# Kernel tuning notes

Measured on AMD Instinct MI355X. Metric: run time of the kernel, lower is better.

## Reference

```python
import jax, jax.numpy as jnp
import numpy as np

H = 1024   # hidden_size
B, S, L = 8, 4096, 64


def setup_inputs() -> dict:
    key = jax.random.key(0)
    k1, k2, k3 = jax.random.split(key, 3)
    hidden = jax.random.normal(k1, (L, B, H), dtype=jnp.float32)
    encoder_states = jax.random.normal(k2, (B, S, 2 * H), dtype=jnp.float32)
    # nn.Linear(2H, H): weight [H, 2H], bias [H]
    W = jax.random.normal(k3, (H, 2 * H), dtype=jnp.float32) * (1.0 / np.sqrt(2 * H))
    b = jnp.zeros((H,), dtype=jnp.float32)
    return {"hidden": hidden, "encoder_states": encoder_states, "W": W, "b": b}


def reference(hidden, encoder_states, W, b):
    # fc projection: [B,S,2H] @ [2H,H] -> [B,S,H]
    reduced = jnp.einsum('bsk,hk->bsh', encoder_states, W) + b
    # scores: bmm(reduced [B,S,H], hidden.permute(1,2,0) [B,H,L]) -> [B,S,L]
    scores = jnp.einsum('bsh,lbh->bsl', reduced, hidden)
    # softmax over encoder positions (dim=1)
    weights = jax.nn.softmax(scores, axis=1)
    # context: bmm(weights^T [B,L,S], reduced [B,S,H]) -> [B,L,H]
    context = jnp.einsum('bsl,bsh->blh', weights, reduced)
    return context, weights
```

## Files before the change

### kernel.cpp

```cpp
#include <hip/hip_runtime.h>


#define H_ 1024
#define B_ 8
#define S_ 4096
#define L_ 64
#define K2H 2048

typedef _Float16 f16x8 __attribute__((ext_vector_type(8)));
typedef _Float16 f16x4 __attribute__((ext_vector_type(4)));
typedef float f32x4 __attribute__((ext_vector_type(4)));


__global__ __launch_bounds__(256) void kcast_kernel(const float* __restrict__ src,
                                                    _Float16* __restrict__ hi,
                                                    _Float16* __restrict__ lo) {
    __shared__ float T[16][516];
    const int t = threadIdx.x;
    const int slab = blockIdx.x, ksec = blockIdx.y;
    const float* sp = src + (size_t)slab * 16 * K2H + ksec * 512;
#pragma unroll
    for (int r = 0; r < 8; r++) {
        int lin = r * 1024 + t * 4;
        int row = lin >> 9, col = lin & 511;
        float4 v = *(const float4*)(sp + (size_t)row * K2H + col);
        T[row][col] = v.x; T[row][col + 1] = v.y; T[row][col + 2] = v.z; T[row][col + 3] = v.w;
    }
    __syncthreads();
    const size_t obase = ((size_t)slab * 64 + ksec * 16) * 512;
#pragma unroll
    for (int r = 0; r < 4; r++) {
        int c = r * 256 + t;
        int kt = c >> 6, lam = c & 63;
        int m = lam & 15, kb = kt * 32 + (lam >> 4) * 8;
        f16x8 h, l;
#pragma unroll
        for (int e = 0; e < 8; e++) {
            float x = T[m][kb + e];
            _Float16 hh = (_Float16)x;
            h[e] = hh;
            l[e] = (_Float16)(x - (float)hh);
        }
        *(f16x8*)(hi + obase + (size_t)c * 8) = h;
        if (lo) *(f16x8*)(lo + obase + (size_t)c * 8) = l;
    }
}

__global__ __launch_bounds__(256, 4) void kcs_kernel(const float* __restrict__ enc,
                                                     _Float16* __restrict__ encB,
                                                     const _Float16* __restrict__ vh,
                                                     const _Float16* __restrict__ vl,
                                                     float* __restrict__ scores) {
    __shared__ _Float16 TT[2][16][520];
    const int t = threadIdx.x;
    const int slab = blockIdx.x;
    const int b = slab >> 8;
    const int w = t >> 6, lane = t & 63;
    const int ml = lane & 15, q = lane >> 4;
    f32x4 acc[4] = {};

    const float* sp0 = enc + (size_t)slab * (16 * K2H);
    float4 rbuf[8];
#pragma unroll
    for (int r = 0; r < 8; r++) {
        int lin = r * 1024 + t * 4;
        rbuf[r] = *(const float4*)(sp0 + (size_t)(lin >> 9) * K2H + (lin & 511));
    }
    const int qb = (slab & 1) * 2;
    const int st = (slab & 255) >> 1;

    for (int ksec = 0; ksec < 4; ksec++) {
#pragma unroll
        for (int r = 0; r < 8; r++) {
            int lin = r * 1024 + t * 4;
            int row = lin >> 9, col = lin & 511;
            float4 v = rbuf[r];
            f16x4 h4, l4;
            h4[0] = (_Float16)v.x; h4[1] = (_Float16)v.y;
            h4[2] = (_Float16)v.z; h4[3] = (_Float16)v.w;
            l4[0] = (_Float16)(v.x - (float)h4[0]);
            l4[1] = (_Float16)(v.y - (float)h4[1]);
            l4[2] = (_Float16)(v.z - (float)h4[2]);
            l4[3] = (_Float16)(v.w - (float)h4[3]);
            *(f16x4*)&TT[0][row][col] = h4;
            *(f16x4*)&TT[1][row][col] = l4;
        }
        __syncthreads();
        if (ksec < 3) {
            const float* sp = sp0 + (ksec + 1) * 512;
#pragma unroll
            for (int r = 0; r < 8; r++) {
                int lin = r * 1024 + t * 4;
                rbuf[r] = *(const float4*)(sp + (size_t)(lin >> 9) * K2H + (lin & 511));
            }
        }
#pragma unroll
        for (int p = 0; p < 4; p++) {
            const int pid = p * 256 + t;
            const int ctl = pid >> 5;
            const int w5 = pid & 31;
            const int oct = w5 >> 4, c = w5 & 15;
            f16x8 v;
#pragma unroll
            for (int e = 0; e < 8; e++) v[e] = TT[0][oct * 8 + e][ctl * 16 + c];
            const int ctg = ksec * 32 + ctl;
            const size_t off = (((size_t)(b * 128 + ctg)) * 128 + st) * 512
                             + (size_t)((qb + oct) * 16 + c) * 8;
            *(f16x8*)(encB + off) = v;
        }
#pragma unroll
        for (int r = 0; r < 4; r++) {
            const int ktl = r * 4 + w;
            const int kb = ktl * 32 + q * 8;
            f16x8 h = *(const f16x8*)&TT[0][ml][kb];
            f16x8 l = *(const f16x8*)&TT[1][ml][kb];
            const int ktg = ksec * 16 + ktl;
            const size_t vbase = (((size_t)(b * 4) * 64) + ktg) * 512 + (size_t)lane * 8;
#pragma unroll
            for (int lt = 0; lt < 4; lt++) {
                f16x8 bH = *(const f16x8*)(vh + vbase + (size_t)lt * 32768);
                f16x8 bL = *(const f16x8*)(vl + vbase + (size_t)lt * 32768);
                acc[lt] = __builtin_amdgcn_mfma_f32_16x16x32_f16(h, bH, acc[lt], 0, 0, 0);
                acc[lt] = __builtin_amdgcn_mfma_f32_16x16x32_f16(l, bH, acc[lt], 0, 0, 0);
                acc[lt] = __builtin_amdgcn_mfma_f32_16x16x32_f16(h, bL, acc[lt], 0, 0, 0);
            }
        }
        __syncthreads();
    }
    float (*P)[16][66] = reinterpret_cast<float (*)[16][66]>(&TT[0][0][0]);
#pragma unroll
    for (int lt = 0; lt < 4; lt++)
#pragma unroll
        for (int r = 0; r < 4; r++)
            P[w][q * 4 + r][lt * 16 + ml] = acc[lt][r];
    __syncthreads();
    const int s0 = (slab & 255) * 16;
#pragma unroll
    for (int u = 0; u < 4; u++) {
        const int idx = u * 256 + t;
        const int srow = idx >> 6, l = idx & 63;
        float v = P[0][srow][l] + P[1][srow][l] + P[2][srow][l] + P[3][srow][l];
        scores[(size_t)b * (S_ * L_) + (size_t)(s0 + srow) * L_ + l] = v;
    }
}

__global__ __launch_bounds__(256) void kv2_kernel(const float* __restrict__ hidden,
                                                  const float* __restrict__ W,
                                                  _Float16* __restrict__ vh,
                                                  _Float16* __restrict__ vl) {
    __shared__ float Ah[64][17];
    __shared__ float Wt[16][64];
    const int b = blockIdx.x;
    const int k0 = blockIdx.y * 64;
    const int t = threadIdx.x;
    const int lt = t & 15, kt = t >> 4;
    float acc[4][4];
#pragma unroll
    for (int i = 0; i < 4; i++)
#pragma unroll
        for (int j = 0; j < 4; j++) acc[i][j] = 0.f;

    const int ar = t >> 2, ac4 = (t & 3) * 4;
    const int wrow = t >> 4, wc4 = (t & 15) * 4;

    for (int h0 = 0; h0 < H_; h0 += 16) {
        float4 av = *(const float4*)(hidden + (size_t)ar * (B_ * H_) + b * H_ + h0 + ac4);
        Ah[ar][ac4 + 0] = av.x; Ah[ar][ac4 + 1] = av.y; Ah[ar][ac4 + 2] = av.z; Ah[ar][ac4 + 3] = av.w;
        *(float4*)&Wt[wrow][wc4] = *(const float4*)(W + (size_t)(h0 + wrow) * K2H + k0 + wc4);
        __syncthreads();
#pragma unroll
        for (int hh = 0; hh < 16; hh++) {
            float a0 = Ah[lt * 4 + 0][hh], a1 = Ah[lt * 4 + 1][hh];
            float a2 = Ah[lt * 4 + 2][hh], a3 = Ah[lt * 4 + 3][hh];
            float4 wv = *(const float4*)&Wt[hh][kt * 4];
            acc[0][0] += a0 * wv.x; acc[0][1] += a0 * wv.y; acc[0][2] += a0 * wv.z; acc[0][3] += a0 * wv.w;
            acc[1][0] += a1 * wv.x; acc[1][1] += a1 * wv.y; acc[1][2] += a1 * wv.z; acc[1][3] += a1 * wv.w;
            acc[2][0] += a2 * wv.x; acc[2][1] += a2 * wv.y; acc[2][2] += a2 * wv.z; acc[2][3] += a2 * wv.w;
            acc[3][0] += a3 * wv.x; acc[3][1] += a3 * wv.y; acc[3][2] += a3 * wv.z; acc[3][3] += a3 * wv.w;
        }
        __syncthreads();
    }
#pragma unroll
    for (int i = 0; i < 4; i++) {
        const int l = lt * 4 + i;
        const int ltile = l >> 4, lam = l & 15;
#pragma unroll
        for (int j = 0; j < 4; j++) {
            const int k = k0 + kt * 4 + j;
            const size_t idx = (((size_t)(b * 4 + ltile) * 64) + (k >> 5)) * 512
                             + (size_t)((((k >> 3) & 3) * 16 + lam) * 8 + (k & 7));
            float v = acc[i][j];
            _Float16 hh = (_Float16)v;
            vh[idx] = hh;
            vl[idx] = (_Float16)(v - (float)hh);
        }
    }
}

__global__ __launch_bounds__(256) void kU_kernel(const _Float16* __restrict__ wa,
                                                 const _Float16* __restrict__ encB,
                                                 float* __restrict__ Upart) {
    const int t = threadIdx.x;
    const int b = blockIdx.x, nc = blockIdx.y, ks = blockIdx.z;
    const int w = t >> 6, lane = t & 63;
    const int ml = lane & 15, q = lane >> 4;
    const int wm = w >> 1, wn = w & 1;
    f32x4 acc[2][2] = {};

    for (int it = 0; it < 32; ++it) {
        const int stile = ks * 32 + it;
        f16x8 bf[2];
#pragma unroll
        for (int j = 0; j < 2; j++) {
            const int ct = nc * 4 + wn * 2 + j;
            bf[j] = *(const f16x8*)(encB + (((size_t)(b * 128 + ct)) * 128 + stile) * 512
                                     + (size_t)lane * 8);
        }
#pragma unroll
        for (int i = 0; i < 2; i++) {
            f16x8 a = *(const f16x8*)(wa + (((size_t)(b * 4 + wm * 2 + i)) * 128 + stile) * 512
                                       + (size_t)lane * 8);
#pragma unroll
            for (int j = 0; j < 2; j++)
                acc[i][j] = __builtin_amdgcn_mfma_f32_16x16x32_f16(a, bf[j], acc[i][j], 0, 0, 0);
        }
    }
#pragma unroll
    for (int i = 0; i < 2; i++)
#pragma unroll
        for (int j = 0; j < 2; j++)
#pragma unroll
            for (int r = 0; r < 4; r++) {
                const int l = wm * 32 + i * 16 + q * 4 + r;
                const int ch = nc * 64 + (wn * 2 + j) * 16 + ml;
                Upart[(((size_t)(ks * 8 + b)) * 64 + l) * K2H + ch] = acc[i][j][r];
            }
}

__global__ __launch_bounds__(256) void kC_kernel(const float* __restrict__ Upart,
                                                 const _Float16* __restrict__ w16h,
                                                 const _Float16* __restrict__ w16l,
                                                 const float* __restrict__ bias,
                                                 float* __restrict__ ctx) {
    __shared__ _Float16 AsH[64][40], AsL[64][40];
    const int t = threadIdx.x;
    const int hc = blockIdx.x, b = blockIdx.y, kq = blockIdx.z;
    const int w = t >> 6, lane = t & 63;
    const int ml = lane & 15, q = lane >> 4;
    const int wm = w >> 1, wn = w & 1;
    f32x4 acc[2][2] = {};
    const int r0 = t >> 2, c8 = (t & 3) * 8;

    for (int k0 = kq * 512; k0 < kq * 512 + 512; k0 += 32) {
        float xv[8];
#pragma unroll
        for (int e = 0; e < 8; e++) xv[e] = 0.f;
        const size_t ub = ((size_t)b * 64 + r0) * K2H + k0 + c8;
#pragma unroll
        for (int p = 0; p < 4; p++) {
            const float* up = Upart + (size_t)p * (8 * 64 * K2H) + ub;
            float4 u0 = *(const float4*)up, u1 = *(const float4*)(up + 4);
            xv[0] += u0.x; xv[1] += u0.y; xv[2] += u0.z; xv[3] += u0.w;
            xv[4] += u1.x; xv[5] += u1.y; xv[6] += u1.z; xv[7] += u1.w;
        }
        f16x8 hh, ll;
#pragma unroll
        for (int e = 0; e < 8; e++) {
            _Float16 hv = (_Float16)xv[e];
            hh[e] = hv;
            ll[e] = (_Float16)(xv[e] - (float)hv);
        }
        *(f16x8*)&AsH[r0][c8] = hh;
        *(f16x8*)&AsL[r0][c8] = ll;
        __syncthreads();
        const int kt = k0 >> 5;
        f16x8 bH[2], bL[2];
#pragma unroll
        for (int j = 0; j < 2; j++) {
            const size_t wb = (((size_t)(hc * 4 + wn * 2 + j)) * 64 + kt) * 512 + (size_t)lane * 8;
            bH[j] = *(const f16x8*)(w16h + wb);
            bL[j] = *(const f16x8*)(w16l + wb);
        }
#pragma unroll
        for (int i = 0; i < 2; i++) {
            f16x8 aH = *(const f16x8*)&AsH[wm * 32 + i * 16 + ml][q * 8];
            f16x8 aL = *(const f16x8*)&AsL[wm * 32 + i * 16 + ml][q * 8];
#pragma unroll
            for (int j = 0; j < 2; j++) {
                acc[i][j] = __builtin_amdgcn_mfma_f32_16x16x32_f16(aH, bH[j], acc[i][j], 0, 0, 0);
                acc[i][j] = __builtin_amdgcn_mfma_f32_16x16x32_f16(aL, bH[j], acc[i][j], 0, 0, 0);
                acc[i][j] = __builtin_amdgcn_mfma_f32_16x16x32_f16(aH, bL[j], acc[i][j], 0, 0, 0);
            }
        }
        __syncthreads();
    }
#pragma unroll
    for (int i = 0; i < 2; i++)
#pragma unroll
        for (int j = 0; j < 2; j++) {
            const int h = hc * 64 + wn * 32 + j * 16 + ml;
            const float bv = (kq == 0) ? bias[h] : 0.f;
#pragma unroll
            for (int r = 0; r < 4; r++) {
                const int l = wm * 32 + i * 16 + q * 4 + r;
                atomicAdd(ctx + (((size_t)(b * 64 + l)) << 10) + h, acc[i][j][r] + bv);
            }
        }
}


__global__ __launch_bounds__(256) void ksb_kernel(const float* __restrict__ hidden,
                                                  const float* __restrict__ bias,
                                                  float* __restrict__ sb) {
    const int b = blockIdx.x, t = threadIdx.x;
    const int l = t & 63, j = t >> 6;
    const float* hp = hidden + (size_t)l * (B_ * H_) + b * H_ + j * 256;
    const float* bp = bias + j * 256;
    float s = 0.f;
    for (int i = 0; i < 64; i++) {
        float4 h4 = *(const float4*)(hp + i * 4);
        float4 b4 = *(const float4*)(bp + i * 4);
        s += h4.x * b4.x + h4.y * b4.y + h4.z * b4.z + h4.w * b4.w;
    }
    __shared__ float red[256];
    red[t] = s; __syncthreads();
    if (t < 128) red[t] += red[t + 128];
    __syncthreads();
    if (t < 64) sb[b * 64 + t] = red[t] + red[t + 64];
}

__global__ __launch_bounds__(256) void kv_kernel(const float* __restrict__ hidden,
                                                 const float* __restrict__ W,
                                                 float* __restrict__ V) {
    __shared__ float Ah[64][17];
    __shared__ float Wt[16][64];
    const int b = blockIdx.x;
    const int k0 = blockIdx.y * 64;
    const int t = threadIdx.x;
    const int lt = t & 15, kt = t >> 4;
    float acc[4][4];
#pragma unroll
    for (int i = 0; i < 4; i++)
#pragma unroll
        for (int j = 0; j < 4; j++) acc[i][j] = 0.f;

    const int ar = t >> 2, ac4 = (t & 3) * 4;
    const int wrow = t >> 4, wc4 = (t & 15) * 4;

    for (int h0 = 0; h0 < H_; h0 += 16) {
        float4 av = *(const float4*)(hidden + (size_t)ar * (B_ * H_) + b * H_ + h0 + ac4);
        Ah[ar][ac4 + 0] = av.x; Ah[ar][ac4 + 1] = av.y; Ah[ar][ac4 + 2] = av.z; Ah[ar][ac4 + 3] = av.w;
        *(float4*)&Wt[wrow][wc4] = *(const float4*)(W + (size_t)(h0 + wrow) * K2H + k0 + wc4);
        __syncthreads();
#pragma unroll
        for (int hh = 0; hh < 16; hh++) {
            float a0 = Ah[lt * 4 + 0][hh], a1 = Ah[lt * 4 + 1][hh];
            float a2 = Ah[lt * 4 + 2][hh], a3 = Ah[lt * 4 + 3][hh];
            float4 wv = *(const float4*)&Wt[hh][kt * 4];
            acc[0][0] += a0 * wv.x; acc[0][1] += a0 * wv.y; acc[0][2] += a0 * wv.z; acc[0][3] += a0 * wv.w;
            acc[1][0] += a1 * wv.x; acc[1][1] += a1 * wv.y; acc[1][2] += a1 * wv.z; acc[1][3] += a1 * wv.w;
            acc[2][0] += a2 * wv.x; acc[2][1] += a2 * wv.y; acc[2][2] += a2 * wv.z; acc[2][3] += a2 * wv.w;
            acc[3][0] += a3 * wv.x; acc[3][1] += a3 * wv.y; acc[3][2] += a3 * wv.z; acc[3][3] += a3 * wv.w;
        }
        __syncthreads();
    }
#pragma unroll
    for (int i = 0; i < 4; i++) {
        float4 o; o.x = acc[i][0]; o.y = acc[i][1]; o.z = acc[i][2]; o.w = acc[i][3];
        *(float4*)(V + (size_t)b * (L_ * K2H) + (lt * 4 + i) * K2H + k0 + kt * 4) = o;
    }
}

__global__ __launch_bounds__(256) void k1_kernel(const float* __restrict__ enc,
                                                 const float* __restrict__ W,
                                                 const float* __restrict__ bias,
                                                 _Float16* __restrict__ reduced) {
    __shared__ _Float16 As[128][40];
    __shared__ _Float16 Bs[128][40];
    const int t = threadIdx.x;
    const int n0 = blockIdx.x * 128;
    const int m0 = blockIdx.y * 128;
    const int w = t >> 6, lane = t & 63;
    const int wr = w >> 1, wc = w & 1;
    const int ml = lane & 15, q = lane >> 4;

    f32x4 acc[4][4];
#pragma unroll
    for (int i = 0; i < 4; i++)
#pragma unroll
        for (int j = 0; j < 4; j++) acc[i][j] = (f32x4){0.f, 0.f, 0.f, 0.f};

    const int r0 = t >> 2;
    const int c8 = (t & 3) * 8;

    for (int k0 = 0; k0 < K2H; k0 += 32) {
#pragma unroll
        for (int j = 0; j < 2; ++j) {
            const int row = r0 + 64 * j;
            const float* pa = enc + (size_t)(m0 + row) * K2H + k0 + c8;
            float4 a0 = *(const float4*)pa, a1 = *(const float4*)(pa + 4);
            f16x8 ha;
            ha[0] = (_Float16)a0.x; ha[1] = (_Float16)a0.y; ha[2] = (_Float16)a0.z; ha[3] = (_Float16)a0.w;
            ha[4] = (_Float16)a1.x; ha[5] = (_Float16)a1.y; ha[6] = (_Float16)a1.z; ha[7] = (_Float16)a1.w;
            *(f16x8*)&As[row][c8] = ha;
            const float* pb = W + (size_t)(n0 + row) * K2H + k0 + c8;
            float4 b0 = *(const float4*)pb, b1 = *(const float4*)(pb + 4);
            f16x8 hb;
            hb[0] = (_Float16)b0.x; hb[1] = (_Float16)b0.y; hb[2] = (_Float16)b0.z; hb[3] = (_Float16)b0.w;
            hb[4] = (_Float16)b1.x; hb[5] = (_Float16)b1.y; hb[6] = (_Float16)b1.z; hb[7] = (_Float16)b1.w;
            *(f16x8*)&Bs[row][c8] = hb;
        }
        __syncthreads();
        f16x8 af[4], bf[4];
#pragma unroll
        for (int i = 0; i < 4; i++) af[i] = *(const f16x8*)&As[wr * 64 + i * 16 + ml][q * 8];
#pragma unroll
        for (int j = 0; j < 4; j++) bf[j] = *(const f16x8*)&Bs[wc * 64 + j * 16 + ml][q * 8];
#pragma unroll
        for (int i = 0; i < 4; i++)
#pragma unroll
            for (int j = 0; j < 4; j++)
                acc[i][j] = __builtin_amdgcn_mfma_f32_16x16x32_f16(af[i], bf[j], acc[i][j], 0, 0, 0);
        __syncthreads();
    }
#pragma unroll
    for (int j = 0; j < 4; j++) {
        const int h = n0 + wc * 64 + j * 16 + ml;
        const float bv = bias[h];
#pragma unroll
        for (int i = 0; i < 4; i++) {
            const int srow = m0 + wr * 64 + i * 16 + q * 4;
#pragma unroll
            for (int r = 0; r < 4; r++)
                reduced[(size_t)(srow + r) * H_ + h] = (_Float16)(acc[i][j][r] + bv);
        }
    }
}

__global__ __launch_bounds__(256) void ks_kernel(const float* __restrict__ enc,
                                                 const float* __restrict__ V,
                                                 const float* __restrict__ sb,
                                                 float* __restrict__ scores) {
    __shared__ _Float16 AsH[64][40], AsL[64][40];
    __shared__ _Float16 BsH[64][40], BsL[64][40];
    const int t = threadIdx.x;
    const int s0 = blockIdx.x * 64;
    const int b = blockIdx.y;
    const int w = t >> 6, lane = t & 63;
    const int ml = lane & 15, q = lane >> 4;

    f32x4 acc[4];
#pragma unroll
    for (int j = 0; j < 4; j++) acc[j] = (f32x4){0.f, 0.f, 0.f, 0.f};

    const int r0 = t >> 2, c8 = (t & 3) * 8;

    for (int k0 = 0; k0 < K2H; k0 += 32) {
        {
            const float* pa = enc + (size_t)(b * S_ + s0 + r0) * K2H + k0 + c8;
            float4 a0 = *(const float4*)pa, a1 = *(const float4*)(pa + 4);
            float xv[8] = {a0.x, a0.y, a0.z, a0.w, a1.x, a1.y, a1.z, a1.w};
            f16x8 hh, ll;
#pragma unroll
            for (int e = 0; e < 8; e++) {
                _Float16 hi = (_Float16)xv[e];
                hh[e] = hi;
                ll[e] = (_Float16)(xv[e] - (float)hi);
            }
            *(f16x8*)&AsH[r0][c8] = hh;
            *(f16x8*)&AsL[r0][c8] = ll;
        }
        {
            const float* pb = V + (size_t)b * (L_ * K2H) + (size_t)r0 * K2H + k0 + c8;
            float4 b0 = *(const float4*)pb, b1 = *(const float4*)(pb + 4);
            float xv[8] = {b0.x, b0.y, b0.z, b0.w, b1.x, b1.y, b1.z, b1.w};
            f16x8 hh, ll;
#pragma unroll
            for (int e = 0; e < 8; e++) {
                _Float16 hi = (_Float16)xv[e];
                hh[e] = hi;
                ll[e] = (_Float16)(xv[e] - (float)hi);
            }
            *(f16x8*)&BsH[r0][c8] = hh;
            *(f16x8*)&BsL[r0][c8] = ll;
        }
        __syncthreads();
        f16x8 aH = *(const f16x8*)&AsH[w * 16 + ml][q * 8];
        f16x8 aL = *(const f16x8*)&AsL[w * 16 + ml][q * 8];
#pragma unroll
        for (int j = 0; j < 4; j++) {
            f16x8 bH = *(const f16x8*)&BsH[j * 16 + ml][q * 8];
            f16x8 bL = *(const f16x8*)&BsL[j * 16 + ml][q * 8];
            acc[j] = __builtin_amdgcn_mfma_f32_16x16x32_f16(aH, bH, acc[j], 0, 0, 0);
            acc[j] = __builtin_amdgcn_mfma_f32_16x16x32_f16(aL, bH, acc[j], 0, 0, 0);
            acc[j] = __builtin_amdgcn_mfma_f32_16x16x32_f16(aH, bL, acc[j], 0, 0, 0);
        }
        __syncthreads();
    }
#pragma unroll
    for (int j = 0; j < 4; j++) {
        const int l = j * 16 + ml;
        const float sbv = sb[b * 64 + l];
        const int srow = s0 + w * 16 + q * 4;
#pragma unroll
        for (int r = 0; r < 4; r++)
            scores[(size_t)b * (S_ * L_) + (size_t)(srow + r) * L_ + l] = acc[j][r] + sbv;
    }
}

__global__ __launch_bounds__(256) void k4_kernel(const float* __restrict__ wbuf,
                                                 const _Float16* __restrict__ reduced,
                                                 float* __restrict__ ctx) {
    __shared__ float Ws[64][64];
    __shared__ _Float16 Rs[64][256];
    const int t = threadIdx.x;
    const int b = blockIdx.x, ht = blockIdx.y, sc = blockIdx.z;
    const int h = ht * 256 + t;
    float acc[64];
#pragma unroll
    for (int l = 0; l < 64; l++) acc[l] = 0.f;

    for (int cc = 0; cc < 4; ++cc) {
        const int sbase = sc * 256 + cc * 64;
#pragma unroll
        for (int j = 0; j < 4; j++) {
            int c = t + 256 * j;
            int row = c >> 4, c4 = (c & 15) * 4;
            *(float4*)&Ws[row][c4] =
                *(const float4*)(wbuf + (size_t)b * (S_ * L_) + (size_t)(sbase + row) * L_ + c4);
        }
#pragma unroll
        for (int j = 0; j < 8; j++) {
            int c = t + 256 * j;
            int row = c >> 5, ch = (c & 31) * 8;
            *(uint4*)&Rs[row][ch] =
                *(const uint4*)(reduced + (size_t)(b * S_ + sbase + row) * H_ + ht * 256 + ch);
        }
        __syncthreads();
        for (int ss = 0; ss < 64; ++ss) {
            float r = (float)Rs[ss][t];
            const float4* wr = (const float4*)&Ws[ss][0];
#pragma unroll
            for (int u = 0; u < 16; u++) {
                float4 wv = wr[u];
                acc[u * 4 + 0] += wv.x * r;
                acc[u * 4 + 1] += wv.y * r;
                acc[u * 4 + 2] += wv.z * r;
                acc[u * 4 + 3] += wv.w * r;
            }
        }
        __syncthreads();
    }
#pragma unroll
    for (int l = 0; l < 64; l++)
        atomicAdd(ctx + (size_t)((b * 64 + l) << 10) + h, acc[l]);
}


__global__ __launch_bounds__(256) void k3a_kernel(const float* __restrict__ scores,
                                                  float* __restrict__ partM,
                                                  float* __restrict__ partD) {
    const int b = blockIdx.x, chunk = blockIdx.y;
    const int t = threadIdx.x;
    const int l = t & 63, si = t >> 6;
    const float* p = scores + (size_t)b * (S_ * L_) + (size_t)(chunk * 256 + si * 64) * L_ + l;
    float m = -__builtin_inff(), d = 0.f;
    for (int i = 0; i < 64; i++) {
        float x = p[i * 64];
        if (x > m) { d = d * __expf(m - x) + 1.f; m = x; }
        else d += __expf(x - m);
    }
    __shared__ float sm[256], sd[256];
    sm[t] = m; sd[t] = d; __syncthreads();
    if (t < 128) {
        float m2 = sm[t + 128], d2 = sd[t + 128];
        if (m2 > sm[t]) { sd[t] = sd[t] * __expf(sm[t] - m2) + d2; sm[t] = m2; }
        else sd[t] += d2 * __expf(m2 - sm[t]);
    }
    __syncthreads();
    if (t < 64) {
        float m1 = sm[t], d1 = sd[t], m2 = sm[t + 64], d2 = sd[t + 64];
        if (m2 > m1) { d1 = d1 * __expf(m1 - m2) + d2; m1 = m2; }
        else d1 += d2 * __expf(m2 - m1);
        partM[(b * 16 + chunk) * 64 + t] = m1;
        partD[(b * 16 + chunk) * 64 + t] = d1;
    }
}

__global__ __launch_bounds__(512) void k3b_kernel(const float* __restrict__ partM,
                                                  const float* __restrict__ partD,
                                                  float* __restrict__ fm,
                                                  float* __restrict__ fdinv) {
    const int t = threadIdx.x;
    const int b = t >> 6, l = t & 63;
    float m = -__builtin_inff(), d = 0.f;
    for (int c = 0; c < 16; c++) {
        float pm = partM[(b * 16 + c) * 64 + l];
        float pd = partD[(b * 16 + c) * 64 + l];
        if (pm > m) { d = d * __expf(m - pm) + pd; m = pm; }
        else d += pd * __expf(pm - m);
    }
    fm[t] = m;
    fdinv[t] = 1.0f / d;
}

__global__ __launch_bounds__(256) void k3c_kernel(float* __restrict__ wbuf,
                                                  const float* __restrict__ fm,
                                                  const float* __restrict__ fdinv,
                                                  _Float16* __restrict__ watile) {
    const int t = threadIdx.x;
    const int l = t & 63;
    const int g = blockIdx.x * 4 + (t >> 6);
    const int b = g >> 9;
    const int s0 = (g & 511) * 8;
    const float m = fm[b * 64 + l];
    const float inv = fdinv[b * 64 + l];
    float* wp = wbuf + (size_t)b * (S_ * L_) + (size_t)s0 * L_ + l;
    float y[8];
#pragma unroll
    for (int i = 0; i < 8; i++) y[i] = __expf(wp[i * L_] - m) * inv;
#pragma unroll
    for (int i = 0; i < 8; i++) wp[i * L_] = y[i];
    if (watile) {
        f16x8 o;
#pragma unroll
        for (int i = 0; i < 8; i++) o[i] = (_Float16)y[i];
        const size_t woff = (((size_t)(b * 4 + (l >> 4)) * 128) + (s0 >> 5)) * 512
                          + (size_t)((((s0 >> 3) & 3) * 16 + (l & 15)) * 8);
        *(f16x8*)(watile + woff) = o;
    }
}

extern "C" void kernel_launch(void* const* d_in, const int* in_sizes, int n_in,
                              void* d_out, int out_size, void* d_ws, size_t ws_size,
                              hipStream_t stream) {
    const float* hidden = (const float*)d_in[0];
    const float* enc    = (const float*)d_in[1];
    const float* W      = (const float*)d_in[2];
    const float* bias   = (const float*)d_in[3];

    float* ctx  = (float*)d_out;
    float* wbuf = (float*)d_out + (B_ * L_ * H_);

    char* ws = (char*)d_ws;
    const size_t NEED_FAST = 209784832;

    if (ws_size >= NEED_FAST) {
        _Float16* encB  = (_Float16*)ws;
        float*    Upart = (float*)(ws + 134217728);
        _Float16* w16h  = (_Float16*)(ws + 150994944);
        _Float16* w16l  = (_Float16*)(ws + 155189248);
        _Float16* vh    = (_Float16*)(ws + 159383552);
        _Float16* vl    = (_Float16*)(ws + 161480704);
        _Float16* watile = vh;
        float* partM = (float*)(ws + 163577856);
        float* partD = partM + 8 * 16 * 64;
        float* fm    = partD + 8 * 16 * 64;
        float* fdinv = fm + 512;

        hipMemsetAsync(ctx, 0, (size_t)B_ * L_ * H_ * sizeof(float), stream);
        kv2_kernel<<<dim3(8, 32), 256, 0, stream>>>(hidden, W, vh, vl);
        kcast_kernel<<<dim3(64, 4), 256, 0, stream>>>(W, w16h, w16l);
        kcs_kernel<<<2048, 256, 0, stream>>>(enc, encB, vh, vl, wbuf);
        k3a_kernel<<<dim3(8, 16), 256, 0, stream>>>(wbuf, partM, partD);
        k3b_kernel<<<1, 512, 0, stream>>>(partM, partD, fm, fdinv);
        k3c_kernel<<<1024, 256, 0, stream>>>(wbuf, fm, fdinv, watile);
        kU_kernel<<<dim3(8, 32, 4), 256, 0, stream>>>(watile, encB, Upart);
        kC_kernel<<<dim3(16, 8, 4), 256, 0, stream>>>(Upart, w16h, w16l, bias, ctx);
    } else {
        _Float16* reduced = (_Float16*)ws;
        float* V     = (float*)(ws + 67108864);
        float* partM = (float*)(ws + 71303168);
        float* partD = partM + 8 * 16 * 64;
        float* fm    = partD + 8 * 16 * 64;
        float* fdinv = fm + 512;
        float* sb    = fdinv + 512;

        hipMemsetAsync(ctx, 0, (size_t)B_ * L_ * H_ * sizeof(float), stream);
        ksb_kernel<<<8, 256, 0, stream>>>(hidden, bias, sb);
        kv_kernel<<<dim3(8, 32), 256, 0, stream>>>(hidden, W, V);
        k1_kernel<<<dim3(8, 256), 256, 0, stream>>>(enc, W, bias, reduced);
        ks_kernel<<<dim3(64, 8), 256, 0, stream>>>(enc, V, sb, wbuf);
        k3a_kernel<<<dim3(8, 16), 256, 0, stream>>>(wbuf, partM, partD);
        k3b_kernel<<<1, 512, 0, stream>>>(partM, partD, fm, fdinv);
        k3c_kernel<<<1024, 256, 0, stream>>>(wbuf, fm, fdinv, (_Float16*)nullptr);
        k4_kernel<<<dim3(8, 4, 16), 256, 0, stream>>>(wbuf, reduced, ctx);
    }
}
```

Measured before the change: 639.0 us.

## Split-K the hidden·W projection across eight H slices with a separate reduce kernel

The kernel that forms hidden·W (the V matrix) is split along the H reduction dimension into eight slices, launching eight times as many blocks. Each block writes its fp32 partial sums to a workspace buffer. A new reduce kernel adds the partials and does the fp16 hi/lo split and tiled store. The aim is to raise occupancy of what was one block per CU with a long serial loop, at the cost of about 33 MB of extra partial-sum traffic and one more kernel launch.

```diff
diff --git a/kernel.cpp b/kernel.cpp
--- a/kernel.cpp
+++ b/kernel.cpp
@@ -144,14 +144,14 @@
     }
 }
 
-__global__ __launch_bounds__(256) void kv2_kernel(const float* __restrict__ hidden,
-                                                  const float* __restrict__ W,
-                                                  _Float16* __restrict__ vh,
-                                                  _Float16* __restrict__ vl) {
+__global__ __launch_bounds__(256) void kv2p_kernel(const float* __restrict__ hidden,
+                                                   const float* __restrict__ W,
+                                                   float* __restrict__ Vpart) {
     __shared__ float Ah[64][17];
     __shared__ float Wt[16][64];
     const int b = blockIdx.x;
     const int k0 = blockIdx.y * 64;
+    const int hq = blockIdx.z;
     const int t = threadIdx.x;
     const int lt = t & 15, kt = t >> 4;
     float acc[4][4];
@@ -163,7 +163,7 @@
     const int ar = t >> 2, ac4 = (t & 3) * 4;
     const int wrow = t >> 4, wc4 = (t & 15) * 4;
 
-    for (int h0 = 0; h0 < H_; h0 += 16) {
+    for (int h0 = hq * 128; h0 < hq * 128 + 128; h0 += 16) {
         float4 av = *(const float4*)(hidden + (size_t)ar * (B_ * H_) + b * H_ + h0 + ac4);
         Ah[ar][ac4 + 0] = av.x; Ah[ar][ac4 + 1] = av.y; Ah[ar][ac4 + 2] = av.z; Ah[ar][ac4 + 3] = av.w;
         *(float4*)&Wt[wrow][wc4] = *(const float4*)(W + (size_t)(h0 + wrow) * K2H + k0 + wc4);
@@ -182,14 +182,36 @@
     }
 #pragma unroll
     for (int i = 0; i < 4; i++) {
-        const int l = lt * 4 + i;
+        float4 o; o.x = acc[i][0]; o.y = acc[i][1]; o.z = acc[i][2]; o.w = acc[i][3];
+        *(float4*)(Vpart + (((size_t)(hq * 8 + b)) * 64 + lt * 4 + i) * K2H + k0 + kt * 4) = o;
+    }
+}
+
+__global__ __launch_bounds__(256) void kvc_kernel(const float* __restrict__ Vpart,
+                                                  _Float16* __restrict__ vh,
+                                                  _Float16* __restrict__ vl) {
+    const int b = blockIdx.x;
+    const int k0 = blockIdx.y * 64;
+    const int t = threadIdx.x;
+#pragma unroll
+    for (int u = 0; u < 4; u++) {
+        const int uid = u * 256 + t;
+        const int l = uid >> 4;
+        const int k4 = (uid & 15) * 4;
+        float4 s = {0.f, 0.f, 0.f, 0.f};
+#pragma unroll
+        for (int hq = 0; hq < 8; hq++) {
+            float4 v = *(const float4*)(Vpart + (((size_t)(hq * 8 + b)) * 64 + l) * K2H + k0 + k4);
+            s.x += v.x; s.y += v.y; s.z += v.z; s.w += v.w;
+        }
+        const float sv[4] = {s.x, s.y, s.z, s.w};
         const int ltile = l >> 4, lam = l & 15;
 #pragma unroll
         for (int j = 0; j < 4; j++) {
-            const int k = k0 + kt * 4 + j;
+            const int k = k0 + k4 + j;
             const size_t idx = (((size_t)(b * 4 + ltile) * 64) + (k >> 5)) * 512
                              + (size_t)((((k >> 3) & 3) * 16 + lam) * 8 + (k & 7));
-            float v = acc[i][j];
+            float v = sv[j];
             _Float16 hh = (_Float16)v;
             vh[idx] = hh;
             vl[idx] = (_Float16)(v - (float)hh);
@@ -652,14 +674,16 @@
         _Float16* w16l  = (_Float16*)(ws + 155189248);
         _Float16* vh    = (_Float16*)(ws + 159383552);
         _Float16* vl    = (_Float16*)(ws + 161480704);
+        float*    Vpart = (float*)(ws + 163577856);
         _Float16* watile = vh;
-        float* partM = (float*)(ws + 163577856);
+        float* partM = (float*)(ws + 197132288);
         float* partD = partM + 8 * 16 * 64;
         float* fm    = partD + 8 * 16 * 64;
         float* fdinv = fm + 512;
 
         hipMemsetAsync(ctx, 0, (size_t)B_ * L_ * H_ * sizeof(float), stream);
-        kv2_kernel<<<dim3(8, 32), 256, 0, stream>>>(hidden, W, vh, vl);
+        kv2p_kernel<<<dim3(8, 32, 8), 256, 0, stream>>>(hidden, W, Vpart);
+        kvc_kernel<<<dim3(8, 32), 256, 0, stream>>>(Vpart, vh, vl);
         kcast_kernel<<<dim3(64, 4), 256, 0, stream>>>(W, w16h, w16l);
         kcs_kernel<<<2048, 256, 0, stream>>>(enc, encB, vh, vl, wbuf);
         k3a_kernel<<<dim3(8, 16), 256, 0, stream>>>(wbuf, partM, partD);
```

After: 598.6 us. 1.07x faster.
